# Optimization experiments

Hardware: AMD Instinct MI355X
Metric: run time of the kernel (lower is better)

The kernel has to match this reference:

```python
import jax, jax.numpy as jnp
import numpy as np

VOCAB, D, L, LT, B = 50000, 300, 256, 8, 256
N_HOPS, N_CLASSES = 6, 3
NEG_INF = -1e9


def setup_inputs() -> dict:
    key = jax.random.key(0)
    ks = jax.random.split(key, 12)
    s = 0.05
    return {
        "embeddings": jax.random.normal(ks[0], (VOCAB, D), jnp.float32) * s,
        "w_lin": jax.random.normal(ks[1], (D, D), jnp.float32) * s,
        "b_lin": jax.random.normal(ks[2], (D,), jnp.float32) * s,
        "w_att": jax.random.normal(ks[3], (2 * D,), jnp.float32) * s,
        "b_att": jax.random.normal(ks[4], (), jnp.float32) * s,
        "w_out": jax.random.normal(ks[5], (D, N_CLASSES), jnp.float32) * s,
        "b_out": jax.random.normal(ks[6], (N_CLASSES,), jnp.float32) * s,
        "context_ids": jax.random.randint(ks[7], (B, L), 0, VOCAB, jnp.int32),
        "context_len": jax.random.randint(ks[8], (B,), 1, L + 1, jnp.int32),
        "target_ids": jax.random.randint(ks[9], (B, LT), 0, VOCAB, jnp.int32),
        "target_len": jax.random.randint(ks[10], (B,), 1, LT + 1, jnp.int32),
        "target_loc": jax.random.randint(ks[11], (B,), 0, L, jnp.int32),
    }


def reference(embeddings, w_lin, b_lin, w_att, b_att, w_out, b_out,
              context_ids, context_len, target_ids, target_len, target_loc):
    # context memory: [B, L, D]
    m = embeddings[context_ids]
    pos = jnp.arange(L)
    mask = pos[None, :] < context_len[:, None]                     # [B, L]
    lens = context_len.astype(jnp.float32)[:, None]
    # absolute distance location vector (model 2): v_i = 1 - |i - loc| / len
    dist = jnp.abs(pos[None, :] - target_loc[:, None]).astype(jnp.float32)
    v_loc = jnp.where(mask, 1.0 - dist / lens, 0.0)                # [B, L]
    ext_mem = m * v_loc[:, :, None]                                # [B, L, D]

    # aspect vector: masked mean of target embeddings -> [B, D]
    tgt = embeddings[target_ids]                                   # [B, LT, D]
    tmask = (jnp.arange(LT)[None, :] < target_len[:, None]).astype(jnp.float32)
    v_aspect = jnp.einsum("btd,bt->bd", tgt, tmask) / target_len.astype(jnp.float32)[:, None]

    vec = v_aspect
    for _ in range(N_HOPS):  # shared weights across hops (AUTO_REUSE)
        linear_out = vec @ w_lin + b_lin                           # [B, D]
        # content attention: score_i = tanh(w_att . [m_i ; v] + b)
        scores = (jnp.einsum("bld,d->bl", ext_mem, w_att[:D])
                  + (vec @ w_att[D:])[:, None] + b_att)
        scores = jnp.tanh(scores)
        alpha = jax.nn.softmax(jnp.where(mask, scores, NEG_INF), axis=-1)
        attn_out = jnp.einsum("bl,bld->bd", alpha, ext_mem)
        vec = attn_out + linear_out

    logits = vec @ w_out + b_out                                   # [B, C]
    return logits
```

## Files before the change

kernel.cpp:

```cpp
#include <hip/hip_runtime.h>

typedef unsigned short u16;
typedef unsigned int   u32;
typedef __fp16 h2t __attribute__((ext_vector_type(2)));

#define D      300
#define L      256
#define LT     8
#define B      256
#define NHOPS  6
#define NCLS   3
#define NT     1024

#define OFF_E    0
#define OFF_VEC  153600
#define OFF_VPK  154848
#define OFF_APK  155808
#define OFF_S0   156384
#define OFF_CTX  157408
#define SMEM_BYTES 158432

#define DPP_ADD(x, ctrl) \
    x += __int_as_float(__builtin_amdgcn_update_dpp(0, __float_as_int(x), ctrl, 0xf, 0xf, true))

__device__ __forceinline__ float dpp_wave_sum(float x) {
    DPP_ADD(x, 0x111);
    DPP_ADD(x, 0x112);
    DPP_ADD(x, 0x114);
    DPP_ADD(x, 0x118);
    DPP_ADD(x, 0x142);
    DPP_ADD(x, 0x143);
    return x;
}
__device__ __forceinline__ float lane63(float x) {
    return __int_as_float(__builtin_amdgcn_readlane(__float_as_int(x), 63));
}
__device__ __forceinline__ u32 pk16(float a, float b) {
    h2t r = __builtin_amdgcn_cvt_pkrtz(a, b);
    return __builtin_bit_cast(u32, r);
}
__device__ __forceinline__ float fdot2(u32 a, u32 b, float c) {
    return __builtin_amdgcn_fdot2(__builtin_bit_cast(h2t, a),
                                  __builtin_bit_cast(h2t, b), c, false);
}

__launch_bounds__(NT, 1)
__global__ void memnet_main(
    const float* __restrict__ emb,
    const float* __restrict__ w_lin,
    const float* __restrict__ b_lin,
    const float* __restrict__ w_att,
    const float* __restrict__ b_att,
    const float* __restrict__ w_out,
    const float* __restrict__ b_out,
    const int* __restrict__ ctx_ids,
    const int* __restrict__ ctx_len,
    const int* __restrict__ tgt_ids,
    const int* __restrict__ tgt_len,
    const int* __restrict__ tgt_loc,
    float* __restrict__ out)
{
    extern __shared__ char sm[];
    float* vec_ = (float*)(sm + OFF_VEC);
    u32*   vpk_ = (u32*)(sm + OFF_VPK);
    u32*   apk_ = (u32*)(sm + OFF_APK);
    float* s0_  = (float*)(sm + OFF_S0);
    int*   ctx_ = (int*)(sm + OFF_CTX);

    const int b = blockIdx.x, t = threadIdx.x;
    const int lane = t & 63, wv = t >> 6;
    const int c  = lane / 5;
    const int qi = lane - 5 * c;
    const int q  = 5 * wv + qi;
    const bool heavy = (wv < 15) && (lane < 60);

    const int clen = ctx_len[b], tlen = tgt_len[b], loc = tgt_loc[b];
    const int lps  = (clen + 1) >> 1;

    const float4 z4 = make_float4(0.f, 0.f, 0.f, 0.f);

    if (t < L) { ctx_[t] = ctx_ids[b * L + t]; s0_[t] = 0.f; }
    if (t >= 300 && t < 312) vec_[t] = 0.f;
    if (t >= 768 && t < 1008) vpk_[t - 768] = 0;
    __syncthreads();

    uint4 wreg[13];
    if (heavy) {
        #pragma unroll
        for (int i = 0; i < 13; ++i) {
            const int k0 = 26 * c + 2 * i;
            float4 w0 = z4, w1 = z4;
            if (k0 < D)     w0 = *(const float4*)(w_lin + (long)k0 * D + 4 * q);
            if (k0 + 1 < D) w1 = *(const float4*)(w_lin + (long)(k0 + 1) * D + 4 * q);
            wreg[i].x = pk16(w0.x, w1.x);
            wreg[i].y = pk16(w0.y, w1.y);
            wreg[i].z = pk16(w0.z, w1.z);
            wreg[i].w = pk16(w0.w, w1.w);
        }
    }

    {
        float4 wa1 = ((const float4*)w_att)[lane];
        float4 wa2 = z4;
        if (lane < 11) wa2 = ((const float4*)w_att)[64 + lane];
        const float rclen = 1.f / (float)clen;
        for (int lp = wv; lp < lps; lp += 16) {
            const int l0 = 2 * lp, l1 = l0 + 1;
            const float4* e0 = (const float4*)(emb + (long)ctx_[l0] * D);
            const float4* e1 = (const float4*)(emb + (long)ctx_[l1] * D);
            const float4 a0 = e0[lane];
            const float4 a1 = e1[lane];
            float4 b0 = z4, b1 = z4;
            if (lane < 11) { b0 = e0[64 + lane]; b1 = e1[64 + lane]; }
            float d0 = a0.x*wa1.x + a0.y*wa1.y + a0.z*wa1.z + a0.w*wa1.w
                     + b0.x*wa2.x + b0.y*wa2.y + b0.z*wa2.z + b0.w*wa2.w;
            float d1 = a1.x*wa1.x + a1.y*wa1.y + a1.z*wa1.z + a1.w*wa1.w
                     + b1.x*wa2.x + b1.y*wa2.y + b1.z*wa2.z + b1.w*wa2.w;
            d0 = dpp_wave_sum(d0);
            d1 = dpp_wave_sum(d1);
            const float vl0 = 1.f - fabsf((float)(l0 - loc)) * rclen;
            const float vl1 = (l1 < clen) ? 1.f - fabsf((float)(l1 - loc)) * rclen : 0.f;
            if (lane == 63) { s0_[l0] = vl0 * d0; s0_[l1] = vl1 * d1; }
            uint4 P;
            P.x = pk16(a0.x * vl0, a1.x * vl1);
            P.y = pk16(a0.y * vl0, a1.y * vl1);
            P.z = pk16(a0.z * vl0, a1.z * vl1);
            P.w = pk16(a0.w * vl0, a1.w * vl1);
            *(uint4*)(sm + OFF_E + (lp * 300 + 4 * lane) * 4) = P;
            if (lane < 11) {
                uint4 Q;
                Q.x = pk16(b0.x * vl0, b1.x * vl1);
                Q.y = pk16(b0.y * vl0, b1.y * vl1);
                Q.z = pk16(b0.z * vl0, b1.z * vl1);
                Q.w = pk16(b0.w * vl0, b1.w * vl1);
                *(uint4*)(sm + OFF_E + (lp * 300 + 256 + 4 * lane) * 4) = Q;
            }
        }
    }

    if (t < D) {
        int ids[LT];
        #pragma unroll
        for (int j = 0; j < LT; ++j) ids[j] = tgt_ids[b * LT + j];
        float s = 0.f;
        #pragma unroll
        for (int j = 0; j < LT; ++j) {
            const int  safe = (j < tlen) ? ids[j] : ids[0];
            const float msk = (j < tlen) ? 1.f : 0.f;
            s += msk * emb[(long)safe * D + t];
        }
        const float v = s / (float)tlen;
        vec_[t] = v;
        const float v2 = __shfl_xor(v, 1);
        if ((t & 1) == 0) {
            const int kp = t >> 1;
            const int cp = kp / 13, sl = kp - 13 * cp;
            vpk_[20 * cp + sl] = pk16(v, v2);
        }
    }

    float4 blin4 = z4;
    if (heavy) blin4 = *(const float4*)(b_lin + 4 * q);
    __syncthreads();

    float4 s0r = z4, wb1 = z4, wb2 = z4;
    float batt = 0.f;
    if (wv == 15) {
        s0r = *(const float4*)(s0_ + 4 * lane);
        wb1 = *(const float4*)(w_att + D + 4 * lane);
        if (lane < 11) wb2 = *(const float4*)(w_att + D + 256 + 4 * lane);
        batt = b_att[0];
    }

    for (int hop = 0; hop < NHOPS; ++hop) {
        float4 acc = z4;
        if (heavy) {
            const uint4* vp4 = (const uint4*)(vpk_ + 20 * c);
            const uint4 V0 = vp4[0], V1 = vp4[1], V2 = vp4[2], V3 = vp4[3];
            const u32 vs[13] = {V0.x, V0.y, V0.z, V0.w,
                                V1.x, V1.y, V1.z, V1.w,
                                V2.x, V2.y, V2.z, V2.w, V3.x};
            #pragma unroll
            for (int i = 0; i < 13; ++i) {
                acc.x = fdot2(vs[i], wreg[i].x, acc.x);
                acc.y = fdot2(vs[i], wreg[i].y, acc.y);
                acc.z = fdot2(vs[i], wreg[i].z, acc.z);
                acc.w = fdot2(vs[i], wreg[i].w, acc.w);
            }
        } else if (wv == 15) {
            __builtin_amdgcn_s_setprio(1);
            const float4 v1 = *(const float4*)(vec_ + 4 * lane);
            float4 v2 = z4;
            if (lane < 11) v2 = *(const float4*)(vec_ + 256 + 4 * lane);
            float p = v1.x*wb1.x + v1.y*wb1.y + v1.z*wb1.z + v1.w*wb1.w
                    + v2.x*wb2.x + v2.y*wb2.y + v2.z*wb2.z + v2.w*wb2.w;
            p = dpp_wave_sum(p);
            const float tb = lane63(p) + batt;
            const int lb = 4 * lane;
            float e0 = 0.f, e1 = 0.f, e2 = 0.f, e3 = 0.f;
            {
                float x, E2, th;
                x = s0r.x + tb; E2 = __expf(2.f * x);
                th = 1.f - 2.f * __builtin_amdgcn_rcpf(E2 + 1.f);
                if (lb + 0 < clen) e0 = __expf(th);
                x = s0r.y + tb; E2 = __expf(2.f * x);
                th = 1.f - 2.f * __builtin_amdgcn_rcpf(E2 + 1.f);
                if (lb + 1 < clen) e1 = __expf(th);
                x = s0r.z + tb; E2 = __expf(2.f * x);
                th = 1.f - 2.f * __builtin_amdgcn_rcpf(E2 + 1.f);
                if (lb + 2 < clen) e2 = __expf(th);
                x = s0r.w + tb; E2 = __expf(2.f * x);
                th = 1.f - 2.f * __builtin_amdgcn_rcpf(E2 + 1.f);
                if (lb + 3 < clen) e3 = __expf(th);
            }
            float es = dpp_wave_sum(e0 + e1 + e2 + e3);
            const float rinv = __builtin_amdgcn_rcpf(lane63(es));
            const int p0 = 2 * lane, p1 = p0 + 1;
            const int c0 = p0 / 11, sl0 = p0 - 11 * c0;
            const int c1 = p1 / 11, sl1 = p1 - 11 * c1;
            apk_[12 * c0 + sl0] = pk16(e0 * rinv, e1 * rinv);
            apk_[12 * c1 + sl1] = pk16(e2 * rinv, e3 * rinv);
            __builtin_amdgcn_s_setprio(0);
        }
        __syncthreads();

        if (heavy) {
            const uint4* ap4 = (const uint4*)(apk_ + 12 * c);
            const uint4 A0 = ap4[0], A1 = ap4[1], A2 = ap4[2];
            const u32 as[12] = {A0.x, A0.y, A0.z, A0.w,
                                A1.x, A1.y, A1.z, A1.w,
                                A2.x, A2.y, A2.z, A2.w};
            const int lp0 = 11 * c;
            const char* ep = sm + OFF_E + (lp0 * 300 + 4 * q) * 4;
            #pragma unroll
            for (int r = 0; r < 11; ++r) {
                if (lp0 + r < lps) {
                    const uint4 e4 = *(const uint4*)(ep + r * 1200);
                    acc.x = fdot2(as[r], e4.x, acc.x);
                    acc.y = fdot2(as[r], e4.y, acc.y);
                    acc.z = fdot2(as[r], e4.z, acc.z);
                    acc.w = fdot2(as[r], e4.w, acc.w);
                }
            }
            float4 s;
            s.x = __shfl(acc.x, lane + 30); s.y = __shfl(acc.y, lane + 30);
            s.z = __shfl(acc.z, lane + 30); s.w = __shfl(acc.w, lane + 30);
            if (c < 6) { acc.x += s.x; acc.y += s.y; acc.z += s.z; acc.w += s.w; }
            s.x = __shfl(acc.x, lane + 15); s.y = __shfl(acc.y, lane + 15);
            s.z = __shfl(acc.z, lane + 15); s.w = __shfl(acc.w, lane + 15);
            if (c < 3) { acc.x += s.x; acc.y += s.y; acc.z += s.z; acc.w += s.w; }
            float4 u1, u2;
            u1.x = __shfl(acc.x, lane + 5);  u1.y = __shfl(acc.y, lane + 5);
            u1.z = __shfl(acc.z, lane + 5);  u1.w = __shfl(acc.w, lane + 5);
            u2.x = __shfl(acc.x, lane + 10); u2.y = __shfl(acc.y, lane + 10);
            u2.z = __shfl(acc.z, lane + 10); u2.w = __shfl(acc.w, lane + 10);
            if (c == 0) {
                float4 nv;
                nv.x = acc.x + u1.x + u2.x + blin4.x;
                nv.y = acc.y + u1.y + u2.y + blin4.y;
                nv.z = acc.z + u1.z + u2.z + blin4.z;
                nv.w = acc.w + u1.w + u2.w + blin4.w;
                *(float4*)(vec_ + 4 * q) = nv;
                const int p0 = 2 * q, p1 = p0 + 1;
                const int ca = p0 / 13, sa = p0 - 13 * ca;
                const int cb = p1 / 13, sb = p1 - 13 * cb;
                vpk_[20 * ca + sa] = pk16(nv.x, nv.y);
                vpk_[20 * cb + sb] = pk16(nv.z, nv.w);
            }
        }
        __syncthreads();
    }

    if (wv < NCLS) {
        float p = 0.f;
        for (int i = lane; i < D; i += 64)
            p += vec_[i] * w_out[i * NCLS + wv];
        p = dpp_wave_sum(p);
        if (lane == 63) out[b * NCLS + wv] = p + b_out[wv];
    }
}

extern "C" void kernel_launch(void* const* d_in, const int* in_sizes, int n_in,
                              void* d_out, int out_size, void* d_ws, size_t ws_size,
                              hipStream_t stream) {
    const float* emb     = (const float*)d_in[0];
    const float* w_lin   = (const float*)d_in[1];
    const float* b_lin   = (const float*)d_in[2];
    const float* w_att   = (const float*)d_in[3];
    const float* b_att   = (const float*)d_in[4];
    const float* w_out   = (const float*)d_in[5];
    const float* b_out   = (const float*)d_in[6];
    const int*   ctx_ids = (const int*)d_in[7];
    const int*   ctx_len = (const int*)d_in[8];
    const int*   tgt_ids = (const int*)d_in[9];
    const int*   tgt_len = (const int*)d_in[10];
    const int*   tgt_loc = (const int*)d_in[11];
    float* out = (float*)d_out;

    (void)hipFuncSetAttribute((const void*)memnet_main,
                              hipFuncAttributeMaxDynamicSharedMemorySize,
                              SMEM_BYTES);
    memnet_main<<<B, NT, SMEM_BYTES, stream>>>(
        emb, w_lin, b_lin, w_att, b_att, w_out, b_out,
        ctx_ids, ctx_len, tgt_ids, tgt_len, tgt_loc, out);
}
```

Baseline: 34.05 us.

## Issue target-embedding loads early and make the context gather branch-free

The target-embedding gather is hoisted ahead of the context-memory build so its global loads overlap with the context gather. The context loop now runs a fixed 8 iterations (unrolled by 2) with clamped indices and zero weights for padded rows, instead of a data-dependent trip count. The extra shared-memory rows and the packed buffers are zero-filled so the attention loop can drop its per-row bounds check. Index arithmetic for the packed-vector writes is also hoisted out of the hop loop. The trade-off is redundant loads and FLOPs for short contexts, plus slightly more shared memory.

Measured after the change: 33.14 us. -2.7%, faster.

```diff
diff --git a/kernel.cpp b/kernel.cpp
--- a/kernel.cpp
+++ b/kernel.cpp
@@ -13,12 +13,12 @@
 #define NT     1024
 
 #define OFF_E    0
-#define OFF_VEC  153600
-#define OFF_VPK  154848
-#define OFF_APK  155808
-#define OFF_S0   156384
-#define OFF_CTX  157408
-#define SMEM_BYTES 158432
+#define OFF_VEC  158400
+#define OFF_VPK  159648
+#define OFF_APK  160608
+#define OFF_S0   161184
+#define OFF_CTX  162208
+#define SMEM_BYTES 163232
 
 #define DPP_ADD(x, ctrl) \
     x += __int_as_float(__builtin_amdgcn_update_dpp(0, __float_as_int(x), ctrl, 0xf, 0xf, true))
@@ -75,14 +75,89 @@
     const bool heavy = (wv < 15) && (lane < 60);
 
     const int clen = ctx_len[b], tlen = tgt_len[b], loc = tgt_loc[b];
-    const int lps  = (clen + 1) >> 1;
 
     const float4 z4 = make_float4(0.f, 0.f, 0.f, 0.f);
 
     if (t < L) { ctx_[t] = ctx_ids[b * L + t]; s0_[t] = 0.f; }
+    if (t < 240) vpk_[t] = 0;
+    if (t < 144) apk_[t] = 0;
     if (t >= 300 && t < 312) vec_[t] = 0.f;
-    if (t >= 768 && t < 1008) vpk_[t - 768] = 0;
+    {
+        u32* ez = (u32*)(sm + OFF_E + 128 * 1200);
+        ez[t] = 0;
+        if (t < 176) ez[1024 + t] = 0;
+    }
     __syncthreads();
+
+    float arow[LT];
+    if (t < D) {
+        int ids[LT];
+        #pragma unroll
+        for (int j = 0; j < LT; ++j) ids[j] = tgt_ids[b * LT + j];
+        #pragma unroll
+        for (int j = 0; j < LT; ++j) {
+            const int safe = (j < tlen) ? ids[j] : ids[0];
+            arow[j] = emb[(long)safe * D + t];
+        }
+    }
+
+    {
+        float4 wa1 = ((const float4*)w_att)[lane];
+        float4 wa2 = z4;
+        if (lane < 11) wa2 = ((const float4*)w_att)[64 + lane];
+        const float rclen = 1.f / (float)clen;
+        #pragma unroll 2
+        for (int it = 0; it < 8; ++it) {
+            const int lp = wv + 16 * it;
+            const int l0 = 2 * lp, l1 = l0 + 1;
+            const int cl0 = (l0 < clen) ? l0 : clen - 1;
+            const int cl1 = (l1 < clen) ? l1 : clen - 1;
+            const float4* e0 = (const float4*)(emb + (long)ctx_[cl0] * D);
+            const float4* e1 = (const float4*)(emb + (long)ctx_[cl1] * D);
+            const float4 a0 = e0[lane];
+            const float4 a1 = e1[lane];
+            float4 b0 = z4, b1 = z4;
+            if (lane < 11) { b0 = e0[64 + lane]; b1 = e1[64 + lane]; }
+            float d0 = a0.x*wa1.x + a0.y*wa1.y + a0.z*wa1.z + a0.w*wa1.w
+                     + b0.x*wa2.x + b0.y*wa2.y + b0.z*wa2.z + b0.w*wa2.w;
+            float d1 = a1.x*wa1.x + a1.y*wa1.y + a1.z*wa1.z + a1.w*wa1.w
+                     + b1.x*wa2.x + b1.y*wa2.y + b1.z*wa2.z + b1.w*wa2.w;
+            d0 = dpp_wave_sum(d0);
+            d1 = dpp_wave_sum(d1);
+            const float vl0 = (l0 < clen) ? 1.f - fabsf((float)(l0 - loc)) * rclen : 0.f;
+            const float vl1 = (l1 < clen) ? 1.f - fabsf((float)(l1 - loc)) * rclen : 0.f;
+            if (lane == 63) { s0_[l0] = vl0 * d0; s0_[l1] = vl1 * d1; }
+            uint4 P;
+            P.x = pk16(a0.x * vl0, a1.x * vl1);
+            P.y = pk16(a0.y * vl0, a1.y * vl1);
+            P.z = pk16(a0.z * vl0, a1.z * vl1);
+            P.w = pk16(a0.w * vl0, a1.w * vl1);
+            *(uint4*)(sm + OFF_E + lp * 1200 + 16 * lane) = P;
+            if (lane < 11) {
+                uint4 Q;
+                Q.x = pk16(b0.x * vl0, b1.x * vl1);
+                Q.y = pk16(b0.y * vl0, b1.y * vl1);
+                Q.z = pk16(b0.z * vl0, b1.z * vl1);
+                Q.w = pk16(b0.w * vl0, b1.w * vl1);
+                *(uint4*)(sm + OFF_E + lp * 1200 + 1024 + 16 * lane) = Q;
+            }
+        }
+    }
+
+    if (t < D) {
+        float s = 0.f;
+        #pragma unroll
+        for (int j = 0; j < LT; ++j)
+            s += (j < tlen) ? arow[j] : 0.f;
+        const float v = s / (float)tlen;
+        vec_[t] = v;
+        const float v2 = __shfl_xor(v, 1);
+        if ((t & 1) == 0) {
+            const int kp = t >> 1;
+            const int cp = kp / 13, sl = kp - 13 * cp;
+            vpk_[20 * cp + sl] = pk16(v, v2);
+        }
+    }
 
     uint4 wreg[13];
     if (heavy) {
@@ -99,87 +174,41 @@
         }
     }
 
-    {
-        float4 wa1 = ((const float4*)w_att)[lane];
-        float4 wa2 = z4;
-        if (lane < 11) wa2 = ((const float4*)w_att)[64 + lane];
-        const float rclen = 1.f / (float)clen;
-        for (int lp = wv; lp < lps; lp += 16) {
-            const int l0 = 2 * lp, l1 = l0 + 1;
-            const float4* e0 = (const float4*)(emb + (long)ctx_[l0] * D);
-            const float4* e1 = (const float4*)(emb + (long)ctx_[l1] * D);
-            const float4 a0 = e0[lane];
-            const float4 a1 = e1[lane];
-            float4 b0 = z4, b1 = z4;
-            if (lane < 11) { b0 = e0[64 + lane]; b1 = e1[64 + lane]; }
-            float d0 = a0.x*wa1.x + a0.y*wa1.y + a0.z*wa1.z + a0.w*wa1.w
-                     + b0.x*wa2.x + b0.y*wa2.y + b0.z*wa2.z + b0.w*wa2.w;
-            float d1 = a1.x*wa1.x + a1.y*wa1.y + a1.z*wa1.z + a1.w*wa1.w
-                     + b1.x*wa2.x + b1.y*wa2.y + b1.z*wa2.z + b1.w*wa2.w;
-            d0 = dpp_wave_sum(d0);
-            d1 = dpp_wave_sum(d1);
-            const float vl0 = 1.f - fabsf((float)(l0 - loc)) * rclen;
-            const float vl1 = (l1 < clen) ? 1.f - fabsf((float)(l1 - loc)) * rclen : 0.f;
-            if (lane == 63) { s0_[l0] = vl0 * d0; s0_[l1] = vl1 * d1; }
-            uint4 P;
-            P.x = pk16(a0.x * vl0, a1.x * vl1);
-            P.y = pk16(a0.y * vl0, a1.y * vl1);
-            P.z = pk16(a0.z * vl0, a1.z * vl1);
-            P.w = pk16(a0.w * vl0, a1.w * vl1);
-            *(uint4*)(sm + OFF_E + (lp * 300 + 4 * lane) * 4) = P;
-            if (lane < 11) {
-                uint4 Q;
-                Q.x = pk16(b0.x * vl0, b1.x * vl1);
-                Q.y = pk16(b0.y * vl0, b1.y * vl1);
-                Q.z = pk16(b0.z * vl0, b1.z * vl1);
-                Q.w = pk16(b0.w * vl0, b1.w * vl1);
-                *(uint4*)(sm + OFF_E + (lp * 300 + 256 + 4 * lane) * 4) = Q;
-            }
-        }
-    }
-
-    if (t < D) {
-        int ids[LT];
-        #pragma unroll
-        for (int j = 0; j < LT; ++j) ids[j] = tgt_ids[b * LT + j];
-        float s = 0.f;
-        #pragma unroll
-        for (int j = 0; j < LT; ++j) {
-            const int  safe = (j < tlen) ? ids[j] : ids[0];
-            const float msk = (j < tlen) ? 1.f : 0.f;
-            s += msk * emb[(long)safe * D + t];
-        }
-        const float v = s / (float)tlen;
-        vec_[t] = v;
-        const float v2 = __shfl_xor(v, 1);
-        if ((t & 1) == 0) {
-            const int kp = t >> 1;
-            const int cp = kp / 13, sl = kp - 13 * cp;
-            vpk_[20 * cp + sl] = pk16(v, v2);
-        }
-    }
-
     float4 blin4 = z4;
     if (heavy) blin4 = *(const float4*)(b_lin + 4 * q);
+
+    int vwa = 0, vwb = 0;
+    if (heavy && c == 0) {
+        const int p0 = 2 * q, p1 = p0 + 1;
+        vwa = 20 * (p0 / 13) + (p0 % 13);
+        vwb = 20 * (p1 / 13) + (p1 % 13);
+    }
     __syncthreads();
 
     float4 s0r = z4, wb1 = z4, wb2 = z4;
     float batt = 0.f;
+    int aw0 = 0, aw1 = 0;
     if (wv == 15) {
         s0r = *(const float4*)(s0_ + 4 * lane);
         wb1 = *(const float4*)(w_att + D + 4 * lane);
         if (lane < 11) wb2 = *(const float4*)(w_att + D + 256 + 4 * lane);
         batt = b_att[0];
-    }
+        const int p0 = 2 * lane, p1 = p0 + 1;
+        aw0 = 12 * (p0 / 11) + (p0 % 11);
+        aw1 = 12 * (p1 / 11) + (p1 % 11);
+    }
+
+    const int lp0 = 11 * c;
 
     for (int hop = 0; hop < NHOPS; ++hop) {
         float4 acc = z4;
         if (heavy) {
             const uint4* vp4 = (const uint4*)(vpk_ + 20 * c);
-            const uint4 V0 = vp4[0], V1 = vp4[1], V2 = vp4[2], V3 = vp4[3];
+            const uint4 V0 = vp4[0], V1 = vp4[1], V2 = vp4[2];
+            const u32 v12 = vpk_[20 * c + 12];
             const u32 vs[13] = {V0.x, V0.y, V0.z, V0.w,
                                 V1.x, V1.y, V1.z, V1.w,
-                                V2.x, V2.y, V2.z, V2.w, V3.x};
+                                V2.x, V2.y, V2.z, V2.w, v12};
             #pragma unroll
             for (int i = 0; i < 13; ++i) {
                 acc.x = fdot2(vs[i], wreg[i].x, acc.x);
@@ -215,11 +244,8 @@
             }
             float es = dpp_wave_sum(e0 + e1 + e2 + e3);
             const float rinv = __builtin_amdgcn_rcpf(lane63(es));
-            const int p0 = 2 * lane, p1 = p0 + 1;
-            const int c0 = p0 / 11, sl0 = p0 - 11 * c0;
-            const int c1 = p1 / 11, sl1 = p1 - 11 * c1;
-            apk_[12 * c0 + sl0] = pk16(e0 * rinv, e1 * rinv);
-            apk_[12 * c1 + sl1] = pk16(e2 * rinv, e3 * rinv);
+            apk_[aw0] = pk16(e0 * rinv, e1 * rinv);
+            apk_[aw1] = pk16(e2 * rinv, e3 * rinv);
             __builtin_amdgcn_s_setprio(0);
         }
         __syncthreads();
@@ -227,20 +253,17 @@
         if (heavy) {
             const uint4* ap4 = (const uint4*)(apk_ + 12 * c);
             const uint4 A0 = ap4[0], A1 = ap4[1], A2 = ap4[2];
-            const u32 as[12] = {A0.x, A0.y, A0.z, A0.w,
+            const u32 as[11] = {A0.x, A0.y, A0.z, A0.w,
                                 A1.x, A1.y, A1.z, A1.w,
-                                A2.x, A2.y, A2.z, A2.w};
-            const int lp0 = 11 * c;
-            const char* ep = sm + OFF_E + (lp0 * 300 + 4 * q) * 4;
+                                A2.x, A2.y, A2.z};
+            const char* ep = sm + OFF_E + lp0 * 1200 + 16 * q;
             #pragma unroll
             for (int r = 0; r < 11; ++r) {
-                if (lp0 + r < lps) {
-                    const uint4 e4 = *(const uint4*)(ep + r * 1200);
-                    acc.x = fdot2(as[r], e4.x, acc.x);
-                    acc.y = fdot2(as[r], e4.y, acc.y);
-                    acc.z = fdot2(as[r], e4.z, acc.z);
-                    acc.w = fdot2(as[r], e4.w, acc.w);
-                }
+                const uint4 e4 = *(const uint4*)(ep + r * 1200);
+                acc.x = fdot2(as[r], e4.x, acc.x);
+                acc.y = fdot2(as[r], e4.y, acc.y);
+                acc.z = fdot2(as[r], e4.z, acc.z);
+                acc.w = fdot2(as[r], e4.w, acc.w);
             }
             float4 s;
             s.x = __shfl(acc.x, lane + 30); s.y = __shfl(acc.y, lane + 30);
@@ -261,11 +284,8 @@
                 nv.z = acc.z + u1.z + u2.z + blin4.z;
                 nv.w = acc.w + u1.w + u2.w + blin4.w;
                 *(float4*)(vec_ + 4 * q) = nv;
-                const int p0 = 2 * q, p1 = p0 + 1;
-                const int ca = p0 / 13, sa = p0 - 13 * ca;
-                const int cb = p1 / 13, sb = p1 - 13 * cb;
-                vpk_[20 * ca + sa] = pk16(nv.x, nv.y);
-                vpk_[20 * cb + sb] = pk16(nv.z, nv.w);
+                vpk_[vwa] = pk16(nv.x, nv.y);
+                vpk_[vwb] = pk16(nv.z, nv.w);
             }
         }
         __syncthreads();
```
